# Kernel tuning notes

Hardware: AMD Instinct MI355X
Metric: run time of the kernel (lower is better)

## Reference

```python
import jax, jax.numpy as jnp
import numpy as np
import math

B, N, IN_DIM, HID, HEADS, K, NCLS = 4, 8192, 1024, 512, 8, 16, 2


def setup_inputs() -> dict:
    key = jax.random.key(0)
    ks = jax.random.split(key, 20)
    s = 0.02
    return {
        "inputs": jax.random.normal(ks[0], (B, N, IN_DIM), jnp.float32),
        "W_feat": jax.random.normal(ks[1], (IN_DIM, HID), jnp.float32) * s,
        "b_feat": jnp.zeros((HID,), jnp.float32),
        "w_enc": jax.random.normal(ks[2], (HID, 1), jnp.float32) * s,
        "b_enc": jnp.zeros((1,), jnp.float32),
        "cls_token": jax.random.normal(ks[3], (1, 1, HID), jnp.float32) * s,
        "conv_w": jax.random.normal(ks[4], (HID, 1, 3, 3), jnp.float32) * s,  # depthwise
        "conv_b": jnp.zeros((HID,), jnp.float32),
        "Wq": jax.random.normal(ks[5], (HID, HID), jnp.float32) * s,
        "bq": jnp.zeros((HID,), jnp.float32),
        "Wk": jax.random.normal(ks[6], (HID, HID), jnp.float32) * s,
        "bk": jnp.zeros((HID,), jnp.float32),
        "Wv": jax.random.normal(ks[7], (HID, HID), jnp.float32) * s,
        "bv": jnp.zeros((HID,), jnp.float32),
        "Wo": jax.random.normal(ks[8], (HID, HID), jnp.float32) * s,
        "bo": jnp.zeros((HID,), jnp.float32),
        "Wc": jax.random.normal(ks[9], (HID, NCLS), jnp.float32) * s,
        "bc": jnp.zeros((NCLS,), jnp.float32),
    }


def reference(inputs, W_feat, b_feat, w_enc, b_enc, cls_token, conv_w, conv_b,
              Wq, bq, Wk, bk, Wv, bv, Wo, bo, Wc, bc):
    # ---- feature projection: [B,N,IN] -> [B,N,HID]
    x = inputs @ W_feat + b_feat

    # ---- recalib(option='max'): sigmoid scores, top-k gather, mean -> Q [B,1,HID]
    scores = jax.nn.sigmoid(jnp.squeeze(x @ w_enc + b_enc, -1))  # [B,N]
    _, idx = jax.lax.top_k(scores, K)                             # [B,K]
    topk = jnp.take_along_axis(x, idx[:, :, None], axis=1)        # [B,K,HID]
    Q = jnp.mean(topk, axis=1, keepdims=True)                     # [B,1,HID]

    # ---- shift + act
    x = jax.nn.relu(x - Q)

    # ---- pad to square grid and run depthwise 3x3 conv with residual
    _H = int(math.ceil(math.sqrt(N)))                             # 91
    add = _H * _H - N
    x = jnp.concatenate([x, x[:, :add]], axis=1)                  # [B, _H*_H, HID]
    feat = jnp.transpose(x, (0, 2, 1)).reshape(B, HID, _H, _H)    # [B,C,H,W]
    conv = jax.lax.conv_general_dilated(
        feat, conv_w, window_strides=(1, 1), padding="SAME",
        feature_group_count=HID)
    feat = conv + conv_b[None, :, None, None] + feat
    x = jnp.transpose(feat.reshape(B, HID, _H * _H), (0, 2, 1))   # [B,_H*_H,HID]

    # ---- prepend cls token
    cls = jnp.broadcast_to(cls_token, (B, 1, HID))
    x = jnp.concatenate([cls, x], axis=1)                         # [B,S,HID]

    # ---- MAB(Q, x): multi-head attention with scale 1/sqrt(dim_V)
    d = HID // HEADS
    q = (Q @ Wq + bq).reshape(B, 1, HEADS, d)
    kk = (x @ Wk + bk).reshape(B, -1, HEADS, d)
    v = (x @ Wv + bv).reshape(B, -1, HEADS, d)
    logits_a = jnp.einsum('bqhd,bkhd->bhqk', q, kk) / math.sqrt(HID)
    A = jax.nn.softmax(logits_a, axis=-1)                         # [B,h,1,S]
    O = q + jnp.einsum('bhqk,bkhd->bqhd', A, v)                   # [B,1,h,d]
    O = O.reshape(B, 1, HID)
    O = O + jax.nn.relu(O @ Wo + bo)
    bag = O[:, 0]                                                 # squeeze(1) -> [B,HID]

    return bag @ Wc + bc                                          # logits [B,NCLS]
```

## Files before the change

kernel.cpp:

```cpp
#include <hip/hip_runtime.h>
#include <hip/hip_bf16.h>
#include <math.h>

#define BB 4
#define NN 8192
#define IND 1024
#define HID 512
#define HEADS 8
#define KSEL 16
#define NCLS 2
#define HH 91
#define NPIX 8281
#define NTOK 8282
#define MROWS 32768

typedef short short8 __attribute__((ext_vector_type(8)));
typedef float floatx4 __attribute__((ext_vector_type(4)));

__device__ __forceinline__ unsigned short f2bf(float f) {
  union { float f; unsigned u; } v; v.f = f;
  unsigned r = (v.u + 0x7FFFu + ((v.u >> 16) & 1u)) >> 16;
  return (unsigned short)r;
}
__device__ __forceinline__ float bf2f(unsigned short h) {
  union { unsigned u; float f; } v; v.u = ((unsigned)h) << 16;
  return v.f;
}
__device__ __forceinline__ unsigned pk_bf16(float a, float b) {
  __hip_bfloat162 h = __float22bfloat162_rn(make_float2(a, b));
  union { __hip_bfloat162 h; unsigned u; } cv; cv.h = h; return cv.u;
}

__device__ __forceinline__ void gld16(const unsigned short* g, void* l) {
  typedef __attribute__((address_space(1))) const void GV;
  typedef __attribute__((address_space(3))) void LV;
  __builtin_amdgcn_global_load_lds((GV*)g, (LV*)l, 16, 0, 0);
}

__global__ void k_wt(const float* __restrict__ W, const float* __restrict__ we,
                     unsigned short* __restrict__ Wt, float* __restrict__ u) {
  __shared__ unsigned short s[64][68];
  int kt = blockIdx.x * 64, nt = blockIdx.y * 64;
  int tid = threadIdx.x;
#pragma unroll
  for (int i = 0; i < 16; ++i) {
    int idx = tid + i * 256;
    int kk2 = idx >> 6, nn2 = idx & 63;
    s[nn2][kk2] = f2bf(W[(long)(kt + kk2) * HID + nt + nn2]);
  }
  __syncthreads();
#pragma unroll
  for (int i = 0; i < 16; ++i) {
    int idx = tid + i * 256;
    int nn2 = idx >> 6, kk2 = idx & 63;
    Wt[(long)(nt + nn2) * IND + kt + kk2] = s[nn2][kk2];
  }
  if (blockIdx.y == 0) {
    int r = tid >> 2, q = tid & 3;
    const float* wr = W + (long)(kt + r) * HID + q * 128;
    const float* wer = we + q * 128;
    float a = 0.f;
#pragma unroll 8
    for (int i = 0; i < 128; ++i) a = fmaf(wr[i], wer[i], a);
    a += __shfl_xor(a, 1);
    a += __shfl_xor(a, 2);
    if (q == 0) u[kt + r] = a;
  }
}

__global__ __launch_bounds__(256) void k_gemm(const float* __restrict__ A,
                                              const unsigned short* __restrict__ Bt,
                                              const float* __restrict__ bias,
                                              const float* __restrict__ u,
                                              unsigned short* __restrict__ X,
                                              float* __restrict__ slog) {
  __shared__ unsigned short sA[2][128 * 32];
  __shared__ unsigned short sB[2][128 * 32];
  __shared__ float su[IND];
  int tid = threadIdx.x;
  int wave = tid >> 6, lane = tid & 63;
  long m0 = (long)blockIdx.x * 128;
  int n0 = blockIdx.y * 128;
  bool do_slog = (blockIdx.y == 0);
  if (do_slog) {
    for (int i = tid; i < IND; i += 256) su[i] = u[i];
  }
  __syncthreads();

  int wm = (wave >> 1) * 64, wn = (wave & 1) * 64;
  int lm = lane & 15, lk = (lane >> 4) * 8;
  floatx4 acc[4][4];
#pragma unroll
  for (int i = 0; i < 4; ++i)
#pragma unroll
    for (int j = 0; j < 4; ++j) acc[i][j] = (floatx4){0.f, 0.f, 0.f, 0.f};

  int arow = tid >> 3;
  int akc = (tid & 7) * 8;
  int aks = akc >> 5;
  int acolin = akc & 31;
  const float* gA = A + (m0 + arow) * (long)IND + akc;
  const unsigned short* gB = Bt + (long)(n0 + (tid >> 2)) * IND + (tid & 3) * 8;
  char* b0d = (char*)sB[0] + wave * 1024;
  char* b1d = (char*)sB[1] + wave * 1024;
  float sacc[4] = {0.f, 0.f, 0.f, 0.f};

  for (int k0 = 0; k0 < IND; k0 += 64) {
    gld16(gB + k0, b0d);
    gld16(gB + k0 + 64 * IND, b0d + 4096);
    gld16(gB + k0 + 32, b1d);
    gld16(gB + k0 + 32 + 64 * IND, b1d + 4096);
#pragma unroll
    for (int i = 0; i < 4; ++i) {
      const float* ap = gA + (long)i * 32 * IND + k0;
      float4 v0 = *(const float4*)ap;
      float4 v1 = *(const float4*)(ap + 4);
      if (do_slog) {
        const float* sk = su + k0 + akc;
        sacc[i] += v0.x * sk[0] + v0.y * sk[1] + v0.z * sk[2] + v0.w * sk[3]
                 + v1.x * sk[4] + v1.y * sk[5] + v1.z * sk[6] + v1.w * sk[7];
      }
      uint4 w;
      w.x = pk_bf16(v0.x, v0.y); w.y = pk_bf16(v0.z, v0.w);
      w.z = pk_bf16(v1.x, v1.y); w.w = pk_bf16(v1.z, v1.w);
      *(uint4*)&sA[aks][(arow + i * 32) * 32 + acolin] = w;
    }
    __syncthreads();
#pragma unroll
    for (int ks = 0; ks < 2; ++ks) {
      short8 af[4], bfr[4];
#pragma unroll
      for (int i = 0; i < 4; ++i)
        af[i] = *(const short8*)(&sA[ks][(wm + i * 16 + lm) * 32 + lk]);
#pragma unroll
      for (int j = 0; j < 4; ++j)
        bfr[j] = *(const short8*)(&sB[ks][(wn + j * 16 + lm) * 32 + lk]);
#pragma unroll
      for (int i = 0; i < 4; ++i)
#pragma unroll
        for (int j = 0; j < 4; ++j)
          acc[i][j] = __builtin_amdgcn_mfma_f32_16x16x32_bf16(af[i], bfr[j], acc[i][j], 0, 0, 0);
    }
    __syncthreads();
  }
  if (do_slog) {
#pragma unroll
    for (int i = 0; i < 4; ++i) {
      float s = sacc[i];
      s += __shfl_xor(s, 1);
      s += __shfl_xor(s, 2);
      s += __shfl_xor(s, 4);
      if ((tid & 7) == 0) slog[m0 + arow + i * 32] = s;
    }
  }
#pragma unroll
  for (int j = 0; j < 4; ++j) {
    int gcol = n0 + wn + j * 16 + lm;
    float bv_ = bias[gcol];
#pragma unroll
    for (int i = 0; i < 4; ++i) {
      long grow = m0 + wm + i * 16 + (lane >> 4) * 4;
#pragma unroll
      for (int r = 0; r < 4; ++r)
        X[(grow + r) * HID + gcol] = f2bf(acc[i][j][r] + bv_);
    }
  }
}

__global__ void k_topa(const float* __restrict__ slog, float* __restrict__ cval,
                       int* __restrict__ cidx) {
  __shared__ float sc[512];
  __shared__ float wv[4];
  __shared__ int wiL[4];
  int b = blockIdx.y, blk = blockIdx.x, tid = threadIdx.x;
  int base = b * NN + blk * 512;
  sc[tid] = slog[base + tid];
  sc[tid + 256] = slog[base + tid + 256];
  __syncthreads();
  int lane = tid & 63, wid = tid >> 6;
  for (int it = 0; it < KSEL; ++it) {
    float v0 = sc[tid], v1 = sc[tid + 256];
    float bv; int bi;
    if (v1 > v0) { bv = v1; bi = tid + 256; } else { bv = v0; bi = tid; }
    for (int off = 32; off; off >>= 1) {
      float v2 = __shfl_down(bv, off);
      int i2 = __shfl_down(bi, off);
      if (v2 > bv || (v2 == bv && i2 < bi)) { bv = v2; bi = i2; }
    }
    if (lane == 0) { wv[wid] = bv; wiL[wid] = bi; }
    __syncthreads();
    if (tid == 0) {
      float best = wv[0]; int besti = wiL[0];
#pragma unroll
      for (int w = 1; w < 4; ++w)
        if (wv[w] > best || (wv[w] == best && wiL[w] < besti)) { best = wv[w]; besti = wiL[w]; }
      cval[(b * 16 + blk) * 16 + it] = best;
      cidx[(b * 16 + blk) * 16 + it] = blk * 512 + besti;
      sc[besti] = -3.4e38f;
    }
    __syncthreads();
  }
}

__global__ void k_topb(const float* __restrict__ cval, const int* __restrict__ cidx,
                       const unsigned short* __restrict__ X, const float* __restrict__ Wq,
                       const float* __restrict__ bq, const float* __restrict__ bk,
                       const float* __restrict__ cls, float* __restrict__ Q,
                       float* __restrict__ qvec, float* __restrict__ bkq,
                       unsigned short* __restrict__ XT) {
  __shared__ float cv[256];
  __shared__ int ci[256];
  __shared__ float wv[4];
  __shared__ int wiL[4];
  __shared__ int wsl[4];
  __shared__ int wi[KSEL];
  __shared__ float sQ[HID];
  __shared__ float sqv[HID];
  int b = blockIdx.x, tid = threadIdx.x;
  cv[tid] = cval[b * 256 + tid];
  ci[tid] = cidx[b * 256 + tid];
  __syncthreads();
  int lane = tid & 63, wid = tid >> 6;
  for (int it = 0; it < KSEL; ++it) {
    float bv = cv[tid]; int bi = ci[tid]; int sl = tid;
    for (int off = 32; off; off >>= 1) {
      float v2 = __shfl_down(bv, off);
      int i2 = __shfl_down(bi, off);
      int s2 = __shfl_down(sl, off);
      if (v2 > bv || (v2 == bv && i2 < bi)) { bv = v2; bi = i2; sl = s2; }
    }
    if (lane == 0) { wv[wid] = bv; wiL[wid] = bi; wsl[wid] = sl; }
    __syncthreads();
    if (tid == 0) {
      float best = wv[0]; int besti = wiL[0]; int bests = wsl[0];
#pragma unroll
      for (int w = 1; w < 4; ++w)
        if (wv[w] > best || (wv[w] == best && wiL[w] < besti)) {
          best = wv[w]; besti = wiL[w]; bests = wsl[w];
        }
      wi[it] = besti;
      cv[bests] = -3.4e38f;
    }
    __syncthreads();
  }
  for (int c = tid; c < HID; c += 256) {
    float s = 0.f;
#pragma unroll
    for (int t2 = 0; t2 < KSEL; ++t2)
      s += bf2f(X[((long)b * NN + wi[t2]) * HID + c]);
    float q = s * (1.f / KSEL);
    Q[b * HID + c] = q;
    sQ[c] = q;
  }
  __syncthreads();
  {
    int c0 = tid, c1 = tid + 256;
    float a0 = 0.f, a1 = 0.f;
#pragma unroll 8
    for (int j = 0; j < HID; ++j) {
      float qj = sQ[j];
      a0 = fmaf(qj, Wq[(long)j * HID + c0], a0);
      a1 = fmaf(qj, Wq[(long)j * HID + c1], a1);
    }
    a0 += bq[c0]; a1 += bq[c1];
    qvec[b * HID + c0] = a0; qvec[b * HID + c1] = a1;
    sqv[c0] = a0; sqv[c1] = a1;
  }
  __syncthreads();
  if (tid < HEADS) {
    float s = 0.f;
#pragma unroll 8
    for (int d = 0; d < 64; ++d) s = fmaf(bk[tid * 64 + d], sqv[tid * 64 + d], s);
    bkq[b * HEADS + tid] = s;
  }
  for (int i = tid; i < HID; i += 256)
    XT[(long)b * NTOK * HID + i] = f2bf(cls[i]);
}

__global__ void k_conv(const unsigned short* __restrict__ X, const float* __restrict__ Q,
                       const float* __restrict__ cw, const float* __restrict__ cb,
                       unsigned short* __restrict__ XT) {
  int tid = threadIdx.x;
  int b = blockIdx.y;
  int c = tid * 2;
  float w0[9], w1[9];
#pragma unroll
  for (int t = 0; t < 9; ++t) { w0[t] = cw[c * 9 + t]; w1[t] = cw[(c + 1) * 9 + t]; }
  float q0 = Q[b * HID + c], q1 = Q[b * HID + c + 1];
  float cb0 = cb[c], cb1 = cb[c + 1];
  int nbase = blockIdx.x * 8;
  const unsigned short* xb = X + (long)b * NN * HID;
#pragma unroll
  for (int ii = 0; ii < 8; ++ii) {
    int n = nbase + ii;
    if (n >= NPIX) break;
    int h = n / HH, w = n - h * HH;
    float a0 = 0.f, a1 = 0.f, c0v = 0.f, c1v = 0.f;
#pragma unroll
    for (int dy = 0; dy < 3; ++dy) {
      int hh2 = h + dy - 1;
      if (hh2 < 0 || hh2 >= HH) continue;
#pragma unroll
      for (int dx = 0; dx < 3; ++dx) {
        int ww2 = w + dx - 1;
        if (ww2 < 0 || ww2 >= HH) continue;
        int n2 = hh2 * HH + ww2;
        int r = n2 < NN ? n2 : n2 - NN;
        unsigned v = *(const unsigned*)(xb + (long)r * HID + c);
        float f0 = bf2f((unsigned short)(v & 0xFFFF));
        float f1 = bf2f((unsigned short)(v >> 16));
        f0 = fmaxf(f0 - q0, 0.f);
        f1 = fmaxf(f1 - q1, 0.f);
        int t = dy * 3 + dx;
        a0 = fmaf(w0[t], f0, a0);
        a1 = fmaf(w1[t], f1, a1);
        if (t == 4) { c0v = f0; c1v = f1; }
      }
    }
    unsigned out = (unsigned)f2bf(a0 + cb0 + c0v) | ((unsigned)f2bf(a1 + cb1 + c1v) << 16);
    *(unsigned*)(XT + ((long)b * NTOK + 1 + n) * HID + c) = out;
  }
}

__global__ void k_tprep(const float* __restrict__ qvec, const float* __restrict__ Wk,
                        float* __restrict__ tmat) {
  __shared__ float qv[HID];
  int b = blockIdx.y, tid = threadIdx.x;
  for (int i = tid; i < HID; i += 256) qv[i] = qvec[b * HID + i];
  __syncthreads();
  int wave = tid >> 6, lane = tid & 63;
  float q8[8];
#pragma unroll
  for (int i = 0; i < 8; ++i) q8[i] = qv[lane * 8 + i];
#pragma unroll
  for (int jj = 0; jj < 4; ++jj) {
    int j = blockIdx.x * 16 + wave * 4 + jj;
    const float* wr = Wk + (long)j * HID + lane * 8;
    float4 a0 = *(const float4*)wr;
    float4 a1 = *(const float4*)(wr + 4);
    float s = a0.x * q8[0] + a0.y * q8[1] + a0.z * q8[2] + a0.w * q8[3] +
              a1.x * q8[4] + a1.y * q8[5] + a1.z * q8[6] + a1.w * q8[7];
#pragma unroll
    for (int off = 1; off < 8; off <<= 1) s += __shfl_xor(s, off);
    if ((lane & 7) == 0)
      tmat[((long)b * HEADS + (lane >> 3)) * HID + j] = s;
  }
}

__global__ void k_logits(const unsigned short* __restrict__ XT, const float* __restrict__ tmat,
                         const float* __restrict__ bkq, float* __restrict__ logits) {
  __shared__ float st[HEADS * HID];
  __shared__ float sb[HEADS];
  int b = blockIdx.y, tid = threadIdx.x;
  for (int i = tid; i < HEADS * HID; i += 256) st[i] = tmat[(long)b * HEADS * HID + i];
  if (tid < HEADS) sb[tid] = bkq[b * HEADS + tid];
  __syncthreads();
  int wave = tid >> 6, lane = tid & 63;
  float tr[HEADS][8];
#pragma unroll
  for (int h = 0; h < HEADS; ++h)
#pragma unroll
    for (int i = 0; i < 8; ++i) tr[h][i] = st[h * HID + lane * 8 + i];
  float sbr[HEADS];
#pragma unroll
  for (int h = 0; h < HEADS; ++h) sbr[h] = sb[h];

  for (long row = blockIdx.x * 4 + wave; row < NTOK; row += 4L * gridDim.x) {
    const unsigned short* xr = XT + ((long)b * NTOK + row) * HID + lane * 8;
    ushort4 v0 = *(const ushort4*)xr;
    ushort4 v1 = *(const ushort4*)(xr + 4);
    float xf[8] = {bf2f(v0.x), bf2f(v0.y), bf2f(v0.z), bf2f(v0.w),
                   bf2f(v1.x), bf2f(v1.y), bf2f(v1.z), bf2f(v1.w)};
    float acc[HEADS];
#pragma unroll
    for (int h = 0; h < HEADS; ++h) {
      float a = 0.f;
#pragma unroll
      for (int i = 0; i < 8; ++i) a = fmaf(xf[i], tr[h][i], a);
      acc[h] = a;
    }
#pragma unroll
    for (int h = 0; h < HEADS; ++h)
      for (int off = 32; off; off >>= 1) acc[h] += __shfl_down(acc[h], off);
    if (lane == 0) {
#pragma unroll
      for (int h = 0; h < HEADS; ++h)
        logits[((long)b * HEADS + h) * NTOK + row] = (acc[h] + sbr[h]) * 0.044194173824159216f;
    }
  }
}

__global__ void k_soft(float* __restrict__ logits, float* __restrict__ wsum) {
  __shared__ float sl[NTOK];
  __shared__ float red[256];
  int bh = blockIdx.x, tid = threadIdx.x;
  for (int i = tid; i < HID; i += 256) wsum[(long)bh * HID + i] = 0.f;
  float* lp = logits + (long)bh * NTOK;
  for (int i = tid; i < NTOK; i += 256) sl[i] = lp[i];
  __syncthreads();
  float m = -3.4e38f;
  for (int i = tid; i < NTOK; i += 256) m = fmaxf(m, sl[i]);
  red[tid] = m; __syncthreads();
  for (int s = 128; s; s >>= 1) { if (tid < s) red[tid] = fmaxf(red[tid], red[tid + s]); __syncthreads(); }
  m = red[0]; __syncthreads();
  float sm = 0.f;
  for (int i = tid; i < NTOK; i += 256) {
    float e = __expf(sl[i] - m);
    sl[i] = e;
    sm += e;
  }
  red[tid] = sm; __syncthreads();
  for (int s = 128; s; s >>= 1) { if (tid < s) red[tid] += red[tid + s]; __syncthreads(); }
  float inv = 1.f / red[0];
  __syncthreads();
  for (int i = tid; i < NTOK; i += 256) lp[i] = sl[i] * inv;
}

__global__ void k_wsum(const unsigned short* __restrict__ XT, const float* __restrict__ P,
                       float* __restrict__ wsum) {
  __shared__ float pw[HEADS * 64];
  int b = blockIdx.y, tid = threadIdx.x;
  int nbase = blockIdx.x * 64;
  for (int i = tid; i < HEADS * 64; i += 256) {
    int h = i >> 6, nn = i & 63;
    long n = nbase + nn;
    pw[i] = (n < NTOK) ? P[((long)b * HEADS + h) * NTOK + n] : 0.f;
  }
  __syncthreads();
  int c = tid * 2;
  float wa[HEADS][2];
#pragma unroll
  for (int h = 0; h < HEADS; ++h) { wa[h][0] = 0.f; wa[h][1] = 0.f; }
  int lim = NTOK - nbase; if (lim > 64) lim = 64;
  for (int nn = 0; nn < lim; ++nn) {
    unsigned v = *(const unsigned*)(XT + ((long)b * NTOK + nbase + nn) * HID + c);
    float f0 = bf2f((unsigned short)(v & 0xFFFF));
    float f1 = bf2f((unsigned short)(v >> 16));
#pragma unroll
    for (int h = 0; h < HEADS; ++h) {
      float p = pw[h * 64 + nn];
      wa[h][0] = fmaf(p, f0, wa[h][0]);
      wa[h][1] = fmaf(p, f1, wa[h][1]);
    }
  }
#pragma unroll
  for (int h = 0; h < HEADS; ++h) {
    atomicAdd(&wsum[((long)b * HEADS + h) * HID + c], wa[h][0]);
    atomicAdd(&wsum[((long)b * HEADS + h) * HID + c + 1], wa[h][1]);
  }
}

__global__ __launch_bounds__(512) void k_ofin(const float* __restrict__ qvec,
                                              const float* __restrict__ wsum,
                                              const float* __restrict__ Wv,
                                              const float* __restrict__ bv,
                                              const float* __restrict__ Wo,
                                              const float* __restrict__ bo,
                                              const float* __restrict__ Wc,
                                              const float* __restrict__ bc,
                                              float* __restrict__ out) {
  __shared__ float sws[HEADS * HID];
  __shared__ float so[HID];
  __shared__ float r0[512], r1[512];
  int b = blockIdx.x, tid = threadIdx.x;
  for (int i = tid; i < HEADS * HID; i += 512) sws[i] = wsum[(long)b * HEADS * HID + i];
  __syncthreads();
  int c = tid;
  const float* wp = sws + (c >> 6) * HID;
  float a = 0.f;
#pragma unroll 8
  for (int j = 0; j < HID; ++j) a = fmaf(wp[j], Wv[(long)j * HID + c], a);
  so[c] = qvec[b * HID + c] + bv[c] + a;
  __syncthreads();
  float a2 = 0.f;
#pragma unroll 8
  for (int j = 0; j < HID; ++j) a2 = fmaf(so[j], Wo[(long)j * HID + c], a2);
  float o2 = so[c] + fmaxf(a2 + bo[c], 0.f);
  r0[tid] = o2 * Wc[c * 2];
  r1[tid] = o2 * Wc[c * 2 + 1];
  __syncthreads();
  for (int s = 256; s; s >>= 1) {
    if (tid < s) { r0[tid] += r0[tid + s]; r1[tid] += r1[tid + s]; }
    __syncthreads();
  }
  if (tid == 0) {
    out[b * NCLS + 0] = r0[0] + bc[0];
    out[b * NCLS + 1] = r1[0] + bc[1];
  }
}

extern "C" void kernel_launch(void* const* d_in, const int* in_sizes, int n_in,
                              void* d_out, int out_size, void* d_ws, size_t ws_size,
                              hipStream_t stream) {
  const float* inputs = (const float*)d_in[0];
  const float* W_feat = (const float*)d_in[1];
  const float* b_feat = (const float*)d_in[2];
  const float* w_enc  = (const float*)d_in[3];
  const float* cls    = (const float*)d_in[5];
  const float* conv_w = (const float*)d_in[6];
  const float* conv_b = (const float*)d_in[7];
  const float* Wq = (const float*)d_in[8];
  const float* bq = (const float*)d_in[9];
  const float* Wk = (const float*)d_in[10];
  const float* bk = (const float*)d_in[11];
  const float* Wv = (const float*)d_in[12];
  const float* bv = (const float*)d_in[13];
  const float* Wo = (const float*)d_in[14];
  const float* bo = (const float*)d_in[15];
  const float* Wc = (const float*)d_in[16];
  const float* bc = (const float*)d_in[17];
  float* out = (float*)d_out;

  char* ws = (char*)d_ws;
  size_t off = 0;
  auto alloc = [&](size_t bytes) -> void* {
    void* p = ws + off;
    off = (off + bytes + 255) & ~(size_t)255;
    return p;
  };
  unsigned short* wt  = (unsigned short*)alloc((size_t)HID * IND * 2);
  unsigned short* X   = (unsigned short*)alloc((size_t)MROWS * HID * 2);
  unsigned short* XT  = (unsigned short*)alloc((size_t)BB * NTOK * HID * 2);
  float* u      = (float*)alloc(IND * 4);
  float* slog   = (float*)alloc((size_t)MROWS * 4);
  float* cvalb  = (float*)alloc(BB * 256 * 4);
  int*   cidxb  = (int*)alloc(BB * 256 * 4);
  float* Q      = (float*)alloc(BB * HID * 4);
  float* qvec   = (float*)alloc(BB * HID * 4);
  float* tmat   = (float*)alloc(BB * HEADS * HID * 4);
  float* bkq    = (float*)alloc(BB * HEADS * 4);
  float* logits = (float*)alloc((size_t)BB * HEADS * NTOK * 4);
  float* wsum   = (float*)alloc(BB * HEADS * HID * 4);

  k_wt<<<dim3(IND / 64, HID / 64), 256, 0, stream>>>(W_feat, w_enc, wt, u);
  k_gemm<<<dim3(MROWS / 128, HID / 128), 256, 0, stream>>>(inputs, wt, b_feat, u, X, slog);
  k_topa<<<dim3(16, BB), 256, 0, stream>>>(slog, cvalb, cidxb);
  k_topb<<<BB, 256, 0, stream>>>(cvalb, cidxb, X, Wq, bq, bk, cls, Q, qvec, bkq, XT);
  k_conv<<<dim3((NPIX + 7) / 8, BB), 256, 0, stream>>>(X, Q, conv_w, conv_b, XT);
  k_tprep<<<dim3(HID / 16, BB), 256, 0, stream>>>(qvec, Wk, tmat);
  k_logits<<<dim3(132, BB), 256, 0, stream>>>(XT, tmat, bkq, logits);
  k_soft<<<BB * HEADS, 256, 0, stream>>>(logits, wsum);
  k_wsum<<<dim3((NTOK + 63) / 64, BB), 256, 0, stream>>>(XT, logits, wsum);
  k_ofin<<<BB, 512, 0, stream>>>(qvec, wsum, Wv, bv, Wo, bo, Wc, bc, out);
}
```

Before: 557.9 us.

## Split fp32->bf16 input conversion and score dot into separate pre-pass kernel

```diff
diff --git a/kernel.cpp b/kernel.cpp
--- a/kernel.cpp
+++ b/kernel.cpp
@@ -1,5 +1,4 @@
 #include <hip/hip_runtime.h>
-#include <hip/hip_bf16.h>
 #include <math.h>
 
 #define BB 4
@@ -26,10 +25,6 @@
   union { unsigned u; float f; } v; v.u = ((unsigned)h) << 16;
   return v.f;
 }
-__device__ __forceinline__ unsigned pk_bf16(float a, float b) {
-  __hip_bfloat162 h = __float22bfloat162_rn(make_float2(a, b));
-  union { __hip_bfloat162 h; unsigned u; } cv; cv.h = h; return cv.u;
-}
 
 __device__ __forceinline__ void gld16(const unsigned short* g, void* l) {
   typedef __attribute__((address_space(1))) const void GV;
@@ -68,25 +63,40 @@
   }
 }
 
-__global__ __launch_bounds__(256) void k_gemm(const float* __restrict__ A,
+__global__ void k_cvt(const float* __restrict__ in, const float* __restrict__ u,
+                      unsigned short* __restrict__ abf, float* __restrict__ slog) {
+  __shared__ float su[IND];
+  int tid = threadIdx.x;
+  for (int i = tid; i < IND; i += 256) su[i] = u[i];
+  __syncthreads();
+  int wave = tid >> 6, lane = tid & 63;
+  long row = (long)blockIdx.x * 4 + wave;
+  const float* ip = in + row * IND;
+  unsigned short* op = abf + row * IND;
+  float acc = 0.f;
+#pragma unroll
+  for (int p = 0; p < 4; ++p) {
+    int k = p * 256 + lane * 4;
+    float4 v = *(const float4*)(ip + k);
+    ushort4 o;
+    o.x = f2bf(v.x); o.y = f2bf(v.y); o.z = f2bf(v.z); o.w = f2bf(v.w);
+    *(ushort4*)(op + k) = o;
+    acc += v.x * su[k] + v.y * su[k + 1] + v.z * su[k + 2] + v.w * su[k + 3];
+  }
+  for (int off = 32; off; off >>= 1) acc += __shfl_down(acc, off);
+  if (lane == 0) slog[row] = acc;
+}
+
+__global__ __launch_bounds__(256) void k_gemm(const unsigned short* __restrict__ A,
                                               const unsigned short* __restrict__ Bt,
                                               const float* __restrict__ bias,
-                                              const float* __restrict__ u,
-                                              unsigned short* __restrict__ X,
-                                              float* __restrict__ slog) {
+                                              unsigned short* __restrict__ X) {
   __shared__ unsigned short sA[2][128 * 32];
   __shared__ unsigned short sB[2][128 * 32];
-  __shared__ float su[IND];
   int tid = threadIdx.x;
   int wave = tid >> 6, lane = tid & 63;
-  long m0 = (long)blockIdx.x * 128;
-  int n0 = blockIdx.y * 128;
-  bool do_slog = (blockIdx.y == 0);
-  if (do_slog) {
-    for (int i = tid; i < IND; i += 256) su[i] = u[i];
-  }
-  __syncthreads();
-
+  long m0 = (long)blockIdx.y * 128;
+  int n0 = blockIdx.x * 128;
   int wm = (wave >> 1) * 64, wn = (wave & 1) * 64;
   int lm = lane & 15, lk = (lane >> 4) * 8;
   floatx4 acc[4][4];
@@ -95,36 +105,22 @@
 #pragma unroll
     for (int j = 0; j < 4; ++j) acc[i][j] = (floatx4){0.f, 0.f, 0.f, 0.f};
 
-  int arow = tid >> 3;
-  int akc = (tid & 7) * 8;
-  int aks = akc >> 5;
-  int acolin = akc & 31;
-  const float* gA = A + (m0 + arow) * (long)IND + akc;
+  const unsigned short* gA = A + (m0 + (tid >> 2)) * IND + (tid & 3) * 8;
   const unsigned short* gB = Bt + (long)(n0 + (tid >> 2)) * IND + (tid & 3) * 8;
-  char* b0d = (char*)sB[0] + wave * 1024;
-  char* b1d = (char*)sB[1] + wave * 1024;
-  float sacc[4] = {0.f, 0.f, 0.f, 0.f};
+  char* a0 = (char*)sA[0] + wave * 1024;
+  char* a1 = (char*)sA[1] + wave * 1024;
+  char* b0 = (char*)sB[0] + wave * 1024;
+  char* b1 = (char*)sB[1] + wave * 1024;
 
   for (int k0 = 0; k0 < IND; k0 += 64) {
-    gld16(gB + k0, b0d);
-    gld16(gB + k0 + 64 * IND, b0d + 4096);
-    gld16(gB + k0 + 32, b1d);
-    gld16(gB + k0 + 32 + 64 * IND, b1d + 4096);
-#pragma unroll
-    for (int i = 0; i < 4; ++i) {
-      const float* ap = gA + (long)i * 32 * IND + k0;
-      float4 v0 = *(const float4*)ap;
-      float4 v1 = *(const float4*)(ap + 4);
-      if (do_slog) {
-        const float* sk = su + k0 + akc;
-        sacc[i] += v0.x * sk[0] + v0.y * sk[1] + v0.z * sk[2] + v0.w * sk[3]
-                 + v1.x * sk[4] + v1.y * sk[5] + v1.z * sk[6] + v1.w * sk[7];
-      }
-      uint4 w;
-      w.x = pk_bf16(v0.x, v0.y); w.y = pk_bf16(v0.z, v0.w);
-      w.z = pk_bf16(v1.x, v1.y); w.w = pk_bf16(v1.z, v1.w);
-      *(uint4*)&sA[aks][(arow + i * 32) * 32 + acolin] = w;
-    }
+    gld16(gA + k0, a0);
+    gld16(gA + k0 + 64 * IND, a0 + 4096);
+    gld16(gA + k0 + 32, a1);
+    gld16(gA + k0 + 32 + 64 * IND, a1 + 4096);
+    gld16(gB + k0, b0);
+    gld16(gB + k0 + 64 * IND, b0 + 4096);
+    gld16(gB + k0 + 32, b1);
+    gld16(gB + k0 + 32 + 64 * IND, b1 + 4096);
     __syncthreads();
 #pragma unroll
     for (int ks = 0; ks < 2; ++ks) {
@@ -142,16 +138,6 @@
           acc[i][j] = __builtin_amdgcn_mfma_f32_16x16x32_bf16(af[i], bfr[j], acc[i][j], 0, 0, 0);
     }
     __syncthreads();
-  }
-  if (do_slog) {
-#pragma unroll
-    for (int i = 0; i < 4; ++i) {
-      float s = sacc[i];
-      s += __shfl_xor(s, 1);
-      s += __shfl_xor(s, 2);
-      s += __shfl_xor(s, 4);
-      if ((tid & 7) == 0) slog[m0 + arow + i * 32] = s;
-    }
   }
 #pragma unroll
   for (int j = 0; j < 4; ++j) {
@@ -518,6 +504,7 @@
     off = (off + bytes + 255) & ~(size_t)255;
     return p;
   };
+  unsigned short* abf = (unsigned short*)alloc((size_t)MROWS * IND * 2);
   unsigned short* wt  = (unsigned short*)alloc((size_t)HID * IND * 2);
   unsigned short* X   = (unsigned short*)alloc((size_t)MROWS * HID * 2);
   unsigned short* XT  = (unsigned short*)alloc((size_t)BB * NTOK * HID * 2);
@@ -533,7 +520,8 @@
   float* wsum   = (float*)alloc(BB * HEADS * HID * 4);
 
   k_wt<<<dim3(IND / 64, HID / 64), 256, 0, stream>>>(W_feat, w_enc, wt, u);
-  k_gemm<<<dim3(MROWS / 128, HID / 128), 256, 0, stream>>>(inputs, wt, b_feat, u, X, slog);
+  k_cvt<<<MROWS / 4, 256, 0, stream>>>(inputs, u, abf, slog);
+  k_gemm<<<dim3(HID / 128, MROWS / 128), 256, 0, stream>>>(abf, wt, b_feat, X);
   k_topa<<<dim3(16, BB), 256, 0, stream>>>(slog, cvalb, cidxb);
   k_topb<<<BB, 256, 0, stream>>>(cvalb, cidxb, X, Wq, bq, bk, cls, Q, qvec, bkq, XT);
   k_conv<<<dim3((NPIX + 7) / 8, BB), 256, 0, stream>>>(X, Q, conv_w, conv_b, XT);
```

Result: no change. 558.2 us (+0.0%).
